# Kernel optimization log

Hardware: AMD Instinct MI355X
Metric: run time of the kernel (lower is better)

The kernel has to match this reference:

```python
import jax, jax.numpy as jnp
import numpy as np

N_NODES = 50000
N_EDGES = 150000
D_FEAT = 512
HIDDEN = 512
N_CLASSES = 47


def gcn_conv(x, edge_index, W, b, n_nodes):
    """PyG GCNConv: out = D^{-1/2} (A + I) D^{-1/2} (x @ W) + b."""
    h = x @ W  # [N, out_dim] dense GEMM
    loop = jnp.arange(n_nodes, dtype=edge_index.dtype)
    row = jnp.concatenate([edge_index[0], loop])  # source
    col = jnp.concatenate([edge_index[1], loop])  # target
    ones = jnp.ones(row.shape[0], dtype=h.dtype)
    deg = jax.ops.segment_sum(ones, col, num_segments=n_nodes)  # in-degree + 1
    dinv = jnp.where(deg > 0, jax.lax.rsqrt(deg), 0.0)
    norm = dinv[row] * dinv[col]  # [E+N]
    msg = norm[:, None] * h[row]  # gather + scale
    out = jax.ops.segment_sum(msg, col, num_segments=n_nodes)  # scatter-add
    return out + b


def setup_inputs() -> dict:
    key = jax.random.key(0)
    k1, k2, k3, k4, k5, k6 = jax.random.split(key, 6)
    x = jax.random.normal(k1, (N_NODES, D_FEAT), dtype=jnp.float32)
    edge_index = jax.random.randint(k2, (2, N_EDGES), 0, N_NODES, dtype=jnp.int64)
    s1 = (6.0 / (D_FEAT + HIDDEN)) ** 0.5
    s2 = (6.0 / (HIDDEN + N_CLASSES)) ** 0.5
    W1 = jax.random.uniform(k3, (D_FEAT, HIDDEN), jnp.float32, -s1, s1)
    b1 = jnp.zeros((HIDDEN,), jnp.float32)
    W2 = jax.random.uniform(k4, (HIDDEN, N_CLASSES), jnp.float32, -s2, s2)
    b2 = jnp.zeros((N_CLASSES,), jnp.float32)
    return {"x": x, "edge_index": edge_index, "W1": W1, "b1": b1, "W2": W2, "b2": b2}


def reference(x, edge_index, W1, b1, W2, b2):
    n = x.shape[0]
    h = gcn_conv(x, edge_index, W1, b1, n)
    h = jax.nn.relu(h)
    # F.dropout(p=0.5, training=self.training): eval mode -> identity
    out = gcn_conv(h, edge_index, W2, b2, n)
    return out
```

## Files before the change

kernel.cpp:

```cpp
#include <hip/hip_runtime.h>
#include <hip/hip_bf16.h>

#define NNODES 50000
#define NEDGES 150000
#define DFEAT  512
#define HID    512
#define NCLS   47

typedef __hip_bfloat16 bf16;
typedef __attribute__((ext_vector_type(8))) short short8;
typedef __attribute__((ext_vector_type(4))) float float4v;

typedef const __attribute__((address_space(1))) unsigned int* gas_t;
typedef __attribute__((address_space(3))) unsigned int* las_t;
__device__ __forceinline__ void load_lds16(const void* g, void* l) {
    __builtin_amdgcn_global_load_lds((gas_t)g, (las_t)l, 16, 0, 0);
}

__device__ __forceinline__ float bfbits_lo(unsigned int w) {
    return __uint_as_float((w & 0xFFFFu) << 16);
}
__device__ __forceinline__ float bfbits_hi(unsigned int w) {
    return __uint_as_float(w & 0xFFFF0000u);
}

__device__ __forceinline__ int eidx(const void* ei, int half, int e, int is64) {
    if (is64) return (int)((const long long*)ei)[(size_t)half * NEDGES + e];
    return ((const int*)ei)[half * NEDGES + e];
}

#define ZB ((NNODES + 255) / 256)
#define PR_W1T (1 + ZB)
#define PR_B1  (PR_W1T + 1024)
#define PR_W2T (PR_B1 + 2)
#define PR_B2  (PR_W2T + 128)
#define PR_GRID (PR_B2 + 1)

__global__ __launch_bounds__(256) void k_prep0(
    const void* x, const void* ei, const void* W1, const void* b1,
    const void* W2, const void* b2, int* flags, unsigned int* cnt,
    bf16* W1T, float* b1c, bf16* W2T, float* b2c) {
    __shared__ int sh[128];
    __shared__ int shflag;
    const int b = blockIdx.x, t = threadIdx.x;

    if (b >= 1 && b < 1 + ZB) {
        int i = (b - 1) * 256 + t;
        if (i < NNODES) cnt[i] = 0u;
        return;
    }

    if (t < 64) {
        const unsigned short* xs = (const unsigned short*)x;
        int c = 0;
        for (int i = t; i < 256; i += 64) {
            unsigned int e = (xs[2 * i] >> 7) & 0xFF;
            c += (e >= 117 && e <= 130) ? 1 : 0;
        }
        sh[t] = c;
        if (b == 0) {
            const int* w = (const int*)ei;
            int o = 0;
            for (int i = 2 * t + 1; i < 512; i += 128) o |= w[i];
            sh[64 + t] = o;
        }
    }
    __syncthreads();
    if (t == 0) {
        int C = 0;
        for (int i = 0; i < 64; i++) C += sh[i];
        shflag = (C > 128) ? 1 : 0;
        if (b == 0) {
            int O = 0;
            for (int i = 0; i < 64; i++) O |= sh[64 + i];
            flags[0] = shflag;
            flags[1] = (O == 0) ? 1 : 0;
        }
    }
    __syncthreads();
    const int isb = shflag;

    if (b == 0) return;

    if (b >= PR_W1T && b < PR_B1) {
        int i = (b - PR_W1T) * 256 + t;
        int k = i / HID, n = i % HID;
        float v = isb ? __bfloat162float(((const bf16*)W1)[i]) : ((const float*)W1)[i];
        W1T[(size_t)n * DFEAT + k] = __float2bfloat16(v);
    } else if (b >= PR_B1 && b < PR_W2T) {
        int i = (b - PR_B1) * 256 + t;
        if (i < HID)
            b1c[i] = isb ? __bfloat162float(((const bf16*)b1)[i]) : ((const float*)b1)[i];
    } else if (b >= PR_W2T && b < PR_B2) {
        int i = (b - PR_W2T) * 256 + t;
        int n = i / HID, k = i % HID;
        float v = 0.0f;
        if (n < NCLS) {
            size_t idx = (size_t)k * NCLS + n;
            v = isb ? __bfloat162float(((const bf16*)W2)[idx]) : ((const float*)W2)[idx];
        }
        W2T[(size_t)n * HID + k] = __float2bfloat16(v);
    } else if (b == PR_B2) {
        if (t < NCLS)
            b2c[t] = isb ? __bfloat162float(((const bf16*)b2)[t]) : ((const float*)b2)[t];
    }
}

__global__ void k_count(const void* ei, int* cnt, const int* flags) {
    int e = blockIdx.x * blockDim.x + threadIdx.x;
    if (e >= NEDGES) return;
    atomicAdd(&cnt[eidx(ei, 1, e, flags[1])], 1);
}

__global__ __launch_bounds__(256) void k_scan_part_dinv(const int* cnt, int* part,
                                                        float* dinv) {
    __shared__ int s[256];
    int i = blockIdx.x * 256 + threadIdx.x;
    int v = (i < NNODES) ? cnt[i] : 0;
    if (i < NNODES) dinv[i] = rsqrtf(1.0f + (float)v);
    s[threadIdx.x] = v;
    __syncthreads();
    for (int off = 128; off > 0; off >>= 1) {
        if (threadIdx.x < off) s[threadIdx.x] += s[threadIdx.x + off];
        __syncthreads();
    }
    if (threadIdx.x == 0) part[blockIdx.x] = s[0];
}

__global__ __launch_bounds__(256) void k_scan_off(int* part, int n) {
    __shared__ int s[256];
    int v = (threadIdx.x < n) ? part[threadIdx.x] : 0;
    s[threadIdx.x] = v;
    __syncthreads();
    for (int off = 1; off < 256; off <<= 1) {
        int t = (threadIdx.x >= off) ? s[threadIdx.x - off] : 0;
        __syncthreads();
        s[threadIdx.x] += t;
        __syncthreads();
    }
    if (threadIdx.x < n) part[threadIdx.x] = s[threadIdx.x] - v;
}

__global__ __launch_bounds__(256) void k_scan_fin(const int* cnt, const int* part,
                                                  int* rowptr, int* cursor) {
    __shared__ int s[256];
    int i = blockIdx.x * 256 + threadIdx.x;
    int v = (i < NNODES) ? cnt[i] : 0;
    s[threadIdx.x] = v;
    __syncthreads();
    for (int off = 1; off < 256; off <<= 1) {
        int t = (threadIdx.x >= off) ? s[threadIdx.x - off] : 0;
        __syncthreads();
        s[threadIdx.x] += t;
        __syncthreads();
    }
    int incl = s[threadIdx.x] + part[blockIdx.x];
    if (i < NNODES) {
        rowptr[i + 1] = incl;
        cursor[i] = incl - v;
    }
    if (i == 0) rowptr[0] = 0;
}

__global__ void k_fill(const void* ei, int* cursor, int* csr_src, const int* flags) {
    int e = blockIdx.x * blockDim.x + threadIdx.x;
    if (e >= NEDGES) return;
    int is64 = flags[1];
    int v = eidx(ei, 1, e, is64);
    int u = eidx(ei, 0, e, is64);
    int pos = atomicAdd(&cursor[v], 1);
    csr_src[pos] = u;
}

__global__ __launch_bounds__(256, 3) void k_gemm1_v3(
    const void* __restrict__ X, const bf16* __restrict__ W1T,
    bf16* __restrict__ h1c, int c0, int C, const int* __restrict__ flags,
    int col_tiles, int rows_per_xcd, int n_row_tiles) {
    const int b = blockIdx.x;
    const int xcd = b & 7;
    const int s = b >> 3;
    const int col_t = s % col_tiles;
    const int lr = s / col_tiles;
    const int row_t = xcd * rows_per_xcd + lr;
    if (row_t >= n_row_tiles) return;

    __shared__ bf16 As[128 * 64];
    __shared__ bf16 Bs[128 * 64];
    const int tid = threadIdx.x;
    const int wave = tid >> 6, lane = tid & 63;
    const int row0 = row_t * 128;
    const int gc0 = c0 + col_t * 128;
    const int isb = flags[0];

    float4v acc[2][8];
#pragma unroll
    for (int i = 0; i < 2; i++)
#pragma unroll
        for (int j = 0; j < 8; j++) acc[i][j] = (float4v){0.f, 0.f, 0.f, 0.f};

    const int rb = wave * 32;
    const int frow = lane & 15;
    const int fk = lane >> 4;

    for (int k0 = 0; k0 < DFEAT; k0 += 64) {
        __syncthreads();
        if (isb) {
            const bf16* xb = (const bf16*)X;
#pragma unroll
            for (int t = 0; t < 4; ++t) {
                int g8 = wave * 4 + t;
                int r = g8 * 8 + (lane >> 3);
                int gr = row0 + r; if (gr >= NNODES) gr = NNODES - 1;
                int ck = (lane & 7) ^ (r & 7);
                load_lds16(xb + (size_t)gr * DFEAT + k0 + ck * 8, &As[g8 * 8 * 64]);
            }
        } else {
            const float* xf = (const float*)X;
            for (int i = tid; i < 128 * 8; i += 256) {
                int r = i >> 3, p = i & 7;
                int gr = row0 + r; if (gr >= NNODES) gr = NNODES - 1;
                int ck = p ^ (r & 7);
                const float* src = xf + (size_t)gr * DFEAT + k0 + ck * 8;
#pragma unroll
                for (int e = 0; e < 8; ++e)
                    As[r * 64 + p * 8 + e] = __float2bfloat16(src[e]);
            }
        }
#pragma unroll
        for (int t = 0; t < 4; ++t) {
            int g8 = wave * 4 + t;
            int cl = g8 * 8 + (lane >> 3);
            int ck = (lane & 7) ^ (cl & 7);
            load_lds16(W1T + (size_t)(gc0 + cl) * DFEAT + k0 + ck * 8, &Bs[g8 * 8 * 64]);
        }
        __syncthreads();
#pragma unroll
        for (int ki = 0; ki < 2; ++ki) {
            const int cc = ki * 4 + fk;
            short8 a[2], b8[8];
#pragma unroll
            for (int i = 0; i < 2; i++) {
                int r = rb + i * 16 + frow;
                a[i] = *(const short8*)&As[r * 64 + (cc ^ (r & 7)) * 8];
            }
#pragma unroll
            for (int j = 0; j < 8; j++) {
                int cl = j * 16 + frow;
                b8[j] = *(const short8*)&Bs[cl * 64 + (cc ^ (cl & 7)) * 8];
            }
#pragma unroll
            for (int i = 0; i < 2; i++)
#pragma unroll
                for (int j = 0; j < 8; j++)
                    acc[i][j] = __builtin_amdgcn_mfma_f32_16x16x32_bf16(a[i], b8[j], acc[i][j], 0, 0, 0);
        }
    }
    const int ccol = gc0 - c0;
#pragma unroll
    for (int i = 0; i < 2; i++) {
#pragma unroll
        for (int r = 0; r < 4; r++) {
            int grow = row0 + rb + i * 16 + (lane >> 4) * 4 + r;
            if (grow < NNODES) {
#pragma unroll
                for (int j = 0; j < 8; j++)
                    h1c[(size_t)grow * C + ccol + j * 16 + (lane & 15)] =
                        __float2bfloat16(acc[i][j][r]);
            }
        }
    }
}

__global__ __launch_bounds__(256) void k_gemm1_mfma(
    const void* __restrict__ X, const bf16* __restrict__ W1T,
    bf16* __restrict__ h1c, int c0, int C, const int* __restrict__ flags) {
    __shared__ bf16 As[128 * 64];
    __shared__ bf16 Bs[64 * 64];
    const int tid = threadIdx.x;
    const int wave = tid >> 6, lane = tid & 63;
    const int row0 = blockIdx.x * 128;
    const int gc0 = c0 + blockIdx.y * 64;
    const int isb = flags[0];
    float4v acc[2][4];
#pragma unroll
    for (int i = 0; i < 2; i++)
#pragma unroll
        for (int j = 0; j < 4; j++) acc[i][j] = (float4v){0.f, 0.f, 0.f, 0.f};
    const int rbase = wave * 32;
    const int fl_row = lane & 15;
    const int fl_k8 = (lane >> 4) * 8;
    for (int k0 = 0; k0 < DFEAT; k0 += 64) {
        __syncthreads();
        if (isb) {
            const bf16* xb = (const bf16*)X;
#pragma unroll
            for (int i = 0; i < 4; ++i) {
                int r = i * 32 + wave * 8;
                int gr = row0 + r + (lane >> 3);
                if (gr >= NNODES) gr = NNODES - 1;
                load_lds16(xb + (size_t)gr * DFEAT + k0 + (lane & 7) * 8, &As[r * 64]);
            }
        } else {
            const float* xf = (const float*)X;
            for (int i = tid; i < 128 * 64; i += 256) {
                int r = i >> 6, c = i & 63;
                int gr = row0 + r;
                if (gr >= NNODES) gr = NNODES - 1;
                As[i] = __float2bfloat16(xf[(size_t)gr * DFEAT + k0 + c]);
            }
        }
#pragma unroll
        for (int i = 0; i < 2; ++i) {
            int r = i * 32 + wave * 8;
            int gn = gc0 + r + (lane >> 3);
            load_lds16(W1T + (size_t)gn * DFEAT + k0 + (lane & 7) * 8, &Bs[r * 64]);
        }
        __syncthreads();
#pragma unroll
        for (int ki = 0; ki < 64; ki += 32) {
            short8 a[2], b[4];
#pragma unroll
            for (int i = 0; i < 2; i++)
                a[i] = *(const short8*)&As[(rbase + i * 16 + fl_row) * 64 + ki + fl_k8];
#pragma unroll
            for (int j = 0; j < 4; j++)
                b[j] = *(const short8*)&Bs[(j * 16 + fl_row) * 64 + ki + fl_k8];
#pragma unroll
            for (int i = 0; i < 2; i++)
#pragma unroll
                for (int j = 0; j < 4; j++)
                    acc[i][j] = __builtin_amdgcn_mfma_f32_16x16x32_bf16(a[i], b[j], acc[i][j], 0, 0, 0);
        }
    }
    const int ccol = blockIdx.y * 64;
#pragma unroll
    for (int i = 0; i < 2; i++) {
#pragma unroll
        for (int r = 0; r < 4; r++) {
            int grow = row0 + rbase + i * 16 + (lane >> 4) * 4 + r;
            if (grow < NNODES) {
#pragma unroll
                for (int j = 0; j < 4; j++)
                    h1c[(size_t)grow * C + ccol + j * 16 + (lane & 15)] =
                        __float2bfloat16(acc[i][j][r]);
            }
        }
    }
}

__global__ __launch_bounds__(256) void k_agg1_512(const bf16* __restrict__ h1c,
                                                  const int* __restrict__ rowptr,
                                                  const int* __restrict__ csr_src,
                                                  const float* __restrict__ dinv,
                                                  const float* __restrict__ b1c,
                                                  bf16* __restrict__ a1c) {
    int v = blockIdx.x * 4 + (threadIdx.x >> 6);
    int lane = threadIdx.x & 63;
    if (v >= NNODES) return;
    int d8 = lane * 8;
    float dv = dinv[v];
    float s2 = dv * dv;
    uint4 w = *(const uint4*)(h1c + (size_t)v * 512 + d8);
    float a0 = s2 * bfbits_lo(w.x), a1 = s2 * bfbits_hi(w.x);
    float a2 = s2 * bfbits_lo(w.y), a3 = s2 * bfbits_hi(w.y);
    float a4 = s2 * bfbits_lo(w.z), a5 = s2 * bfbits_hi(w.z);
    float a6 = s2 * bfbits_lo(w.w), a7 = s2 * bfbits_hi(w.w);
    int pend = rowptr[v + 1];
    for (int p = rowptr[v]; p < pend; ++p) {
        int u = csr_src[p];
        float nw = dinv[u] * dv;
        uint4 q = *(const uint4*)(h1c + (size_t)u * 512 + d8);
        a0 += nw * bfbits_lo(q.x); a1 += nw * bfbits_hi(q.x);
        a2 += nw * bfbits_lo(q.y); a3 += nw * bfbits_hi(q.y);
        a4 += nw * bfbits_lo(q.z); a5 += nw * bfbits_hi(q.z);
        a6 += nw * bfbits_lo(q.w); a7 += nw * bfbits_hi(q.w);
    }
    const float* bb = b1c + d8;
    a0 += bb[0]; a1 += bb[1]; a2 += bb[2]; a3 += bb[3];
    a4 += bb[4]; a5 += bb[5]; a6 += bb[6]; a7 += bb[7];
    bf16 o[8];
    o[0] = __float2bfloat16(a0 > 0.f ? a0 : 0.f);
    o[1] = __float2bfloat16(a1 > 0.f ? a1 : 0.f);
    o[2] = __float2bfloat16(a2 > 0.f ? a2 : 0.f);
    o[3] = __float2bfloat16(a3 > 0.f ? a3 : 0.f);
    o[4] = __float2bfloat16(a4 > 0.f ? a4 : 0.f);
    o[5] = __float2bfloat16(a5 > 0.f ? a5 : 0.f);
    o[6] = __float2bfloat16(a6 > 0.f ? a6 : 0.f);
    o[7] = __float2bfloat16(a7 > 0.f ? a7 : 0.f);
    *(uint4*)(a1c + (size_t)v * 512 + d8) = *(uint4*)o;
}

__global__ __launch_bounds__(256) void k_agg1(const bf16* __restrict__ h1c,
                                              const int* __restrict__ rowptr,
                                              const int* __restrict__ csr_src,
                                              const float* __restrict__ dinv,
                                              const float* __restrict__ b1c, int c0, int C,
                                              bf16* __restrict__ a1c) {
    const int tshift = (C == 512) ? 7 : (C == 256) ? 6 : (C == 128) ? 5 : 4;
    long long gt = (long long)blockIdx.x * 256 + threadIdx.x;
    int v = (int)(gt >> tshift);
    int d4 = (int)((gt & ((1 << tshift) - 1)) << 2);
    if (v >= NNODES) return;
    float dv = dinv[v];
    uint2 w = *(const uint2*)(h1c + (size_t)v * C + d4);
    float s2 = dv * dv;
    float a0 = s2 * bfbits_lo(w.x), a1 = s2 * bfbits_hi(w.x);
    float a2 = s2 * bfbits_lo(w.y), a3 = s2 * bfbits_hi(w.y);
    int pend = rowptr[v + 1];
    for (int p = rowptr[v]; p < pend; ++p) {
        int u = csr_src[p];
        float nw = dinv[u] * dv;
        uint2 q = *(const uint2*)(h1c + (size_t)u * C + d4);
        a0 += nw * bfbits_lo(q.x); a1 += nw * bfbits_hi(q.x);
        a2 += nw * bfbits_lo(q.y); a3 += nw * bfbits_hi(q.y);
    }
    const float* bb = b1c + c0 + d4;
    a0 += bb[0]; a1 += bb[1]; a2 += bb[2]; a3 += bb[3];
    bf16 o[4];
    o[0] = __float2bfloat16(a0 > 0.f ? a0 : 0.f);
    o[1] = __float2bfloat16(a1 > 0.f ? a1 : 0.f);
    o[2] = __float2bfloat16(a2 > 0.f ? a2 : 0.f);
    o[3] = __float2bfloat16(a3 > 0.f ? a3 : 0.f);
    *(uint2*)(a1c + (size_t)v * C + d4) = *(uint2*)o;
}

__global__ __launch_bounds__(128) void k_gemm2_64(
    const bf16* __restrict__ A, int C, const bf16* __restrict__ W2T, int kg0,
    float* __restrict__ h2, int accum) {
    __shared__ bf16 As[64 * 64];
    __shared__ bf16 Bs[64 * 64];
    const int tid = threadIdx.x;
    const int wave = tid >> 6, lane = tid & 63;
    const int row0 = blockIdx.x * 64;
    float4v acc[2][4];
#pragma unroll
    for (int i = 0; i < 2; i++)
#pragma unroll
        for (int j = 0; j < 4; j++) acc[i][j] = (float4v){0.f, 0.f, 0.f, 0.f};
    const int rb = wave * 32;
    const int frow = lane & 15;
    const int fk = lane >> 4;

    for (int kk = 0; kk < C; kk += 64) {
        __syncthreads();
#pragma unroll
        for (int t = 0; t < 4; ++t) {
            int g8 = wave * 4 + t;
            int r = g8 * 8 + (lane >> 3);
            int gr = row0 + r; if (gr >= NNODES) gr = NNODES - 1;
            int ck = (lane & 7) ^ (r & 7);
            load_lds16(A + (size_t)gr * C + kk + ck * 8, &As[g8 * 8 * 64]);
        }
#pragma unroll
        for (int t = 0; t < 4; ++t) {
            int g8 = wave * 4 + t;
            int cl = g8 * 8 + (lane >> 3);
            int ck = (lane & 7) ^ (cl & 7);
            load_lds16(W2T + (size_t)cl * HID + kg0 + kk + ck * 8, &Bs[g8 * 8 * 64]);
        }
        __syncthreads();
#pragma unroll
        for (int ki = 0; ki < 2; ++ki) {
            const int cc = ki * 4 + fk;
            short8 a[2], b8[4];
#pragma unroll
            for (int i = 0; i < 2; i++) {
                int r = rb + i * 16 + frow;
                a[i] = *(const short8*)&As[r * 64 + (cc ^ (r & 7)) * 8];
            }
#pragma unroll
            for (int j = 0; j < 4; j++) {
                int cl = j * 16 + frow;
                b8[j] = *(const short8*)&Bs[cl * 64 + (cc ^ (cl & 7)) * 8];
            }
#pragma unroll
            for (int i = 0; i < 2; i++)
#pragma unroll
                for (int j = 0; j < 4; j++)
                    acc[i][j] = __builtin_amdgcn_mfma_f32_16x16x32_bf16(a[i], b8[j], acc[i][j], 0, 0, 0);
        }
    }
#pragma unroll
    for (int i = 0; i < 2; i++) {
#pragma unroll
        for (int r = 0; r < 4; r++) {
            int grow = row0 + rb + i * 16 + (lane >> 4) * 4 + r;
            if (grow < NNODES) {
#pragma unroll
                for (int j = 0; j < 4; j++) {
                    size_t o = (size_t)grow * 64 + j * 16 + frow;
                    h2[o] = accum ? h2[o] + acc[i][j][r] : acc[i][j][r];
                }
            }
        }
    }
}

__global__ __launch_bounds__(256) void k_agg2(const float* __restrict__ h2,
                                              const int* __restrict__ rowptr,
                                              const int* __restrict__ csr_src,
                                              const float* __restrict__ dinv,
                                              const float* __restrict__ b2c,
                                              void* out, const int* flags) {
    int v = blockIdx.x * 4 + (threadIdx.x >> 6);
    int d = threadIdx.x & 63;
    if (v >= NNODES || d >= NCLS) return;
    float dv = dinv[v];
    float acc = dv * dv * h2[(size_t)v * 64 + d];
    int pend = rowptr[v + 1];
    for (int p = rowptr[v]; p < pend; ++p) {
        int u = csr_src[p];
        acc += dinv[u] * dv * h2[(size_t)u * 64 + d];
    }
    acc += b2c[d];
    size_t o = (size_t)v * NCLS + d;
    if (flags[0]) ((bf16*)out)[o] = __float2bfloat16(acc);
    else          ((float*)out)[o] = acc;
}

extern "C" void kernel_launch(void* const* d_in, const int* in_sizes, int n_in,
                              void* d_out, int out_size, void* d_ws, size_t ws_size,
                              hipStream_t stream) {
    const void* x  = d_in[0];
    const void* ei = d_in[1];
    const void* W1 = d_in[2];
    const void* b1 = d_in[3];
    const void* W2 = d_in[4];
    const void* b2 = d_in[5];

    char* base = (char*)d_ws;
    auto alloc = [&](size_t bytes) -> char* {
        char* p = base;
        base += (bytes + 255) & ~(size_t)255;
        return p;
    };
    int*   flags  = (int*)alloc(64);
    int*   cnt    = (int*)alloc(sizeof(int) * NNODES);
    int*   part   = (int*)alloc(sizeof(int) * 256);
    int*   rowptr = (int*)alloc(sizeof(int) * (NNODES + 1));
    int*   cursor = (int*)alloc(sizeof(int) * NNODES);
    int*   csr    = (int*)alloc(sizeof(int) * NEDGES);
    float* dinv   = (float*)alloc(sizeof(float) * NNODES);
    bf16*  W1T    = (bf16*)alloc(sizeof(bf16) * DFEAT * HID);
    float* b1c    = (float*)alloc(sizeof(float) * HID);
    bf16*  W2T    = (bf16*)alloc(sizeof(bf16) * 64 * HID);
    float* b2c    = (float*)alloc(sizeof(float) * 64);
    float* h2     = (float*)alloc(sizeof(float) * (size_t)NNODES * 64);

    size_t used = (size_t)(base - (char*)d_ws);
    size_t rem = (ws_size > used) ? ws_size - used : 0;
    int C = 64;
    if (rem >= (size_t)200000 * 512 + 1024) C = 512;
    else if (rem >= (size_t)200000 * 256 + 1024) C = 256;
    else if (rem >= (size_t)200000 * 128 + 1024) C = 128;
    bf16* h1c = (bf16*)alloc(sizeof(bf16) * (size_t)NNODES * C);
    bf16* a1c = (bf16*)alloc(sizeof(bf16) * (size_t)NNODES * C);

    k_prep0<<<PR_GRID, 256, 0, stream>>>(x, ei, W1, b1, W2, b2, flags,
                                         (unsigned int*)cnt, W1T, b1c, W2T, b2c);
    k_count<<<(NEDGES + 255) / 256, 256, 0, stream>>>(ei, cnt, flags);
    const int nsb = (NNODES + 255) / 256;
    k_scan_part_dinv<<<nsb, 256, 0, stream>>>(cnt, part, dinv);
    k_scan_off<<<1, 256, 0, stream>>>(part, nsb);
    k_scan_fin<<<nsb, 256, 0, stream>>>(cnt, part, rowptr, cursor);
    k_fill<<<(NEDGES + 255) / 256, 256, 0, stream>>>(ei, cursor, csr, flags);

    const int rowblocks = (NNODES + 127) / 128;
    const int rows_per_xcd = (rowblocks + 7) / 8;
    int chunk_i = 0;
    for (int c0 = 0; c0 < HID; c0 += C, ++chunk_i) {
        if (C >= 128) {
            int col_tiles = C / 128;
            int nblk = 8 * rows_per_xcd * col_tiles;
            k_gemm1_v3<<<nblk, 256, 0, stream>>>(x, W1T, h1c, c0, C, flags,
                                                 col_tiles, rows_per_xcd, rowblocks);
        } else {
            dim3 g1(rowblocks, 1);
            k_gemm1_mfma<<<g1, 256, 0, stream>>>(x, W1T, h1c, c0, C, flags);
        }
        if (C == 512) {
            k_agg1_512<<<(NNODES + 3) / 4, 256, 0, stream>>>(h1c, rowptr, csr, dinv, b1c, a1c);
        } else {
            size_t nthr = (size_t)NNODES * (C / 4);
            k_agg1<<<(int)((nthr + 255) / 256), 256, 0, stream>>>(h1c, rowptr, csr, dinv, b1c, c0, C, a1c);
        }
        k_gemm2_64<<<(NNODES + 63) / 64, 128, 0, stream>>>(a1c, C, W2T, c0, h2, chunk_i > 0 ? 1 : 0);
    }

    k_agg2<<<(NNODES + 3) / 4, 256, 0, stream>>>(h2, rowptr, csr, dinv, b2c, d_out, flags);
}
```

Before: 336.2 us.

## Aggregate input features first, then fuse both GEMMs with bias and ReLU

Uses linearity (A·(XW) = (A·X)W) to run the first sparse aggregation directly on the input features and write a bf16 aggregated matrix. A single fused kernel then computes the first GEMM, adds bias, applies ReLU, stages the hidden tile in LDS and multiplies by W2 immediately. The per-column-tile partial outputs are accumulated into h2 with float atomics, and h2 is zeroed in the prep kernel. This removes the h1/a1 intermediate round trips and several launches, at the cost of atomic contention on h2 and reading fp32 x in the gather.

```diff
diff --git a/kernel.cpp b/kernel.cpp
--- a/kernel.cpp
+++ b/kernel.cpp
@@ -30,7 +30,9 @@
 }
 
 #define ZB ((NNODES + 255) / 256)
-#define PR_W1T (1 + ZB)
+#define NZH2 ((NNODES * 64 / 4 + 255) / 256)
+#define PR_ZH2 (1 + ZB)
+#define PR_W1T (PR_ZH2 + NZH2)
 #define PR_B1  (PR_W1T + 1024)
 #define PR_W2T (PR_B1 + 2)
 #define PR_B2  (PR_W2T + 128)
@@ -39,7 +41,7 @@
 __global__ __launch_bounds__(256) void k_prep0(
     const void* x, const void* ei, const void* W1, const void* b1,
     const void* W2, const void* b2, int* flags, unsigned int* cnt,
-    bf16* W1T, float* b1c, bf16* W2T, float* b2c) {
+    bf16* W1T, float* b1c, bf16* W2T, float* b2c, float* h2) {
     __shared__ int sh[128];
     __shared__ int shflag;
     const int b = blockIdx.x, t = threadIdx.x;
@@ -47,6 +49,12 @@
     if (b >= 1 && b < 1 + ZB) {
         int i = (b - 1) * 256 + t;
         if (i < NNODES) cnt[i] = 0u;
+        return;
+    }
+    if (b >= PR_ZH2 && b < PR_W1T) {
+        int i = (b - PR_ZH2) * 256 + t;
+        if (i < NNODES * 64 / 4)
+            ((float4v*)h2)[i] = (float4v){0.f, 0.f, 0.f, 0.f};
         return;
     }
 
@@ -172,276 +180,90 @@
     csr_src[pos] = u;
 }
 
-__global__ __launch_bounds__(256, 3) void k_gemm1_v3(
-    const void* __restrict__ X, const bf16* __restrict__ W1T,
-    bf16* __restrict__ h1c, int c0, int C, const int* __restrict__ flags,
-    int col_tiles, int rows_per_xcd, int n_row_tiles) {
-    const int b = blockIdx.x;
-    const int xcd = b & 7;
-    const int s = b >> 3;
-    const int col_t = s % col_tiles;
-    const int lr = s / col_tiles;
-    const int row_t = xcd * rows_per_xcd + lr;
-    if (row_t >= n_row_tiles) return;
-
-    __shared__ bf16 As[128 * 64];
-    __shared__ bf16 Bs[128 * 64];
-    const int tid = threadIdx.x;
-    const int wave = tid >> 6, lane = tid & 63;
-    const int row0 = row_t * 128;
-    const int gc0 = c0 + col_t * 128;
-    const int isb = flags[0];
-
-    float4v acc[2][8];
-#pragma unroll
-    for (int i = 0; i < 2; i++)
-#pragma unroll
-        for (int j = 0; j < 8; j++) acc[i][j] = (float4v){0.f, 0.f, 0.f, 0.f};
-
-    const int rb = wave * 32;
-    const int frow = lane & 15;
-    const int fk = lane >> 4;
-
-    for (int k0 = 0; k0 < DFEAT; k0 += 64) {
-        __syncthreads();
-        if (isb) {
-            const bf16* xb = (const bf16*)X;
-#pragma unroll
-            for (int t = 0; t < 4; ++t) {
-                int g8 = wave * 4 + t;
-                int r = g8 * 8 + (lane >> 3);
-                int gr = row0 + r; if (gr >= NNODES) gr = NNODES - 1;
-                int ck = (lane & 7) ^ (r & 7);
-                load_lds16(xb + (size_t)gr * DFEAT + k0 + ck * 8, &As[g8 * 8 * 64]);
-            }
-        } else {
-            const float* xf = (const float*)X;
-            for (int i = tid; i < 128 * 8; i += 256) {
-                int r = i >> 3, p = i & 7;
-                int gr = row0 + r; if (gr >= NNODES) gr = NNODES - 1;
-                int ck = p ^ (r & 7);
-                const float* src = xf + (size_t)gr * DFEAT + k0 + ck * 8;
-#pragma unroll
-                for (int e = 0; e < 8; ++e)
-                    As[r * 64 + p * 8 + e] = __float2bfloat16(src[e]);
-            }
-        }
-#pragma unroll
-        for (int t = 0; t < 4; ++t) {
-            int g8 = wave * 4 + t;
-            int cl = g8 * 8 + (lane >> 3);
-            int ck = (lane & 7) ^ (cl & 7);
-            load_lds16(W1T + (size_t)(gc0 + cl) * DFEAT + k0 + ck * 8, &Bs[g8 * 8 * 64]);
-        }
-        __syncthreads();
-#pragma unroll
-        for (int ki = 0; ki < 2; ++ki) {
-            const int cc = ki * 4 + fk;
-            short8 a[2], b8[8];
-#pragma unroll
-            for (int i = 0; i < 2; i++) {
-                int r = rb + i * 16 + frow;
-                a[i] = *(const short8*)&As[r * 64 + (cc ^ (r & 7)) * 8];
-            }
-#pragma unroll
-            for (int j = 0; j < 8; j++) {
-                int cl = j * 16 + frow;
-                b8[j] = *(const short8*)&Bs[cl * 64 + (cc ^ (cl & 7)) * 8];
-            }
-#pragma unroll
-            for (int i = 0; i < 2; i++)
-#pragma unroll
-                for (int j = 0; j < 8; j++)
-                    acc[i][j] = __builtin_amdgcn_mfma_f32_16x16x32_bf16(a[i], b8[j], acc[i][j], 0, 0, 0);
-        }
-    }
-    const int ccol = gc0 - c0;
-#pragma unroll
-    for (int i = 0; i < 2; i++) {
-#pragma unroll
-        for (int r = 0; r < 4; r++) {
-            int grow = row0 + rb + i * 16 + (lane >> 4) * 4 + r;
-            if (grow < NNODES) {
-#pragma unroll
-                for (int j = 0; j < 8; j++)
-                    h1c[(size_t)grow * C + ccol + j * 16 + (lane & 15)] =
-                        __float2bfloat16(acc[i][j][r]);
-            }
-        }
-    }
-}
-
-__global__ __launch_bounds__(256) void k_gemm1_mfma(
-    const void* __restrict__ X, const bf16* __restrict__ W1T,
-    bf16* __restrict__ h1c, int c0, int C, const int* __restrict__ flags) {
-    __shared__ bf16 As[128 * 64];
-    __shared__ bf16 Bs[64 * 64];
-    const int tid = threadIdx.x;
-    const int wave = tid >> 6, lane = tid & 63;
-    const int row0 = blockIdx.x * 128;
-    const int gc0 = c0 + blockIdx.y * 64;
-    const int isb = flags[0];
-    float4v acc[2][4];
-#pragma unroll
-    for (int i = 0; i < 2; i++)
-#pragma unroll
-        for (int j = 0; j < 4; j++) acc[i][j] = (float4v){0.f, 0.f, 0.f, 0.f};
-    const int rbase = wave * 32;
-    const int fl_row = lane & 15;
-    const int fl_k8 = (lane >> 4) * 8;
-    for (int k0 = 0; k0 < DFEAT; k0 += 64) {
-        __syncthreads();
-        if (isb) {
-            const bf16* xb = (const bf16*)X;
-#pragma unroll
-            for (int i = 0; i < 4; ++i) {
-                int r = i * 32 + wave * 8;
-                int gr = row0 + r + (lane >> 3);
-                if (gr >= NNODES) gr = NNODES - 1;
-                load_lds16(xb + (size_t)gr * DFEAT + k0 + (lane & 7) * 8, &As[r * 64]);
-            }
-        } else {
-            const float* xf = (const float*)X;
-            for (int i = tid; i < 128 * 64; i += 256) {
-                int r = i >> 6, c = i & 63;
-                int gr = row0 + r;
-                if (gr >= NNODES) gr = NNODES - 1;
-                As[i] = __float2bfloat16(xf[(size_t)gr * DFEAT + k0 + c]);
-            }
-        }
-#pragma unroll
-        for (int i = 0; i < 2; ++i) {
-            int r = i * 32 + wave * 8;
-            int gn = gc0 + r + (lane >> 3);
-            load_lds16(W1T + (size_t)gn * DFEAT + k0 + (lane & 7) * 8, &Bs[r * 64]);
-        }
-        __syncthreads();
-#pragma unroll
-        for (int ki = 0; ki < 64; ki += 32) {
-            short8 a[2], b[4];
-#pragma unroll
-            for (int i = 0; i < 2; i++)
-                a[i] = *(const short8*)&As[(rbase + i * 16 + fl_row) * 64 + ki + fl_k8];
-#pragma unroll
-            for (int j = 0; j < 4; j++)
-                b[j] = *(const short8*)&Bs[(j * 16 + fl_row) * 64 + ki + fl_k8];
-#pragma unroll
-            for (int i = 0; i < 2; i++)
-#pragma unroll
-                for (int j = 0; j < 4; j++)
-                    acc[i][j] = __builtin_amdgcn_mfma_f32_16x16x32_bf16(a[i], b[j], acc[i][j], 0, 0, 0);
-        }
-    }
-    const int ccol = blockIdx.y * 64;
-#pragma unroll
-    for (int i = 0; i < 2; i++) {
-#pragma unroll
-        for (int r = 0; r < 4; r++) {
-            int grow = row0 + rbase + i * 16 + (lane >> 4) * 4 + r;
-            if (grow < NNODES) {
-#pragma unroll
-                for (int j = 0; j < 4; j++)
-                    h1c[(size_t)grow * C + ccol + j * 16 + (lane & 15)] =
-                        __float2bfloat16(acc[i][j][r]);
-            }
-        }
-    }
-}
-
-__global__ __launch_bounds__(256) void k_agg1_512(const bf16* __restrict__ h1c,
-                                                  const int* __restrict__ rowptr,
-                                                  const int* __restrict__ csr_src,
-                                                  const float* __restrict__ dinv,
-                                                  const float* __restrict__ b1c,
-                                                  bf16* __restrict__ a1c) {
+__global__ __launch_bounds__(256) void k_aggx(const void* __restrict__ X,
+                                              const int* __restrict__ rowptr,
+                                              const int* __restrict__ csr_src,
+                                              const float* __restrict__ dinv,
+                                              bf16* __restrict__ ax,
+                                              const int* __restrict__ flags) {
     int v = blockIdx.x * 4 + (threadIdx.x >> 6);
     int lane = threadIdx.x & 63;
     if (v >= NNODES) return;
     int d8 = lane * 8;
     float dv = dinv[v];
     float s2 = dv * dv;
-    uint4 w = *(const uint4*)(h1c + (size_t)v * 512 + d8);
-    float a0 = s2 * bfbits_lo(w.x), a1 = s2 * bfbits_hi(w.x);
-    float a2 = s2 * bfbits_lo(w.y), a3 = s2 * bfbits_hi(w.y);
-    float a4 = s2 * bfbits_lo(w.z), a5 = s2 * bfbits_hi(w.z);
-    float a6 = s2 * bfbits_lo(w.w), a7 = s2 * bfbits_hi(w.w);
+    float a0, a1, a2, a3, a4, a5, a6, a7;
     int pend = rowptr[v + 1];
-    for (int p = rowptr[v]; p < pend; ++p) {
-        int u = csr_src[p];
-        float nw = dinv[u] * dv;
-        uint4 q = *(const uint4*)(h1c + (size_t)u * 512 + d8);
-        a0 += nw * bfbits_lo(q.x); a1 += nw * bfbits_hi(q.x);
-        a2 += nw * bfbits_lo(q.y); a3 += nw * bfbits_hi(q.y);
-        a4 += nw * bfbits_lo(q.z); a5 += nw * bfbits_hi(q.z);
-        a6 += nw * bfbits_lo(q.w); a7 += nw * bfbits_hi(q.w);
-    }
-    const float* bb = b1c + d8;
-    a0 += bb[0]; a1 += bb[1]; a2 += bb[2]; a3 += bb[3];
-    a4 += bb[4]; a5 += bb[5]; a6 += bb[6]; a7 += bb[7];
+    if (flags[0]) {
+        const bf16* xb = (const bf16*)X;
+        uint4 w = *(const uint4*)(xb + (size_t)v * 512 + d8);
+        a0 = s2 * bfbits_lo(w.x); a1 = s2 * bfbits_hi(w.x);
+        a2 = s2 * bfbits_lo(w.y); a3 = s2 * bfbits_hi(w.y);
+        a4 = s2 * bfbits_lo(w.z); a5 = s2 * bfbits_hi(w.z);
+        a6 = s2 * bfbits_lo(w.w); a7 = s2 * bfbits_hi(w.w);
+        for (int p = rowptr[v]; p < pend; ++p) {
+            int u = csr_src[p];
+            float nw = dinv[u] * dv;
+            uint4 q = *(const uint4*)(xb + (size_t)u * 512 + d8);
+            a0 += nw * bfbits_lo(q.x); a1 += nw * bfbits_hi(q.x);
+            a2 += nw * bfbits_lo(q.y); a3 += nw * bfbits_hi(q.y);
+            a4 += nw * bfbits_lo(q.z); a5 += nw * bfbits_hi(q.z);
+            a6 += nw * bfbits_lo(q.w); a7 += nw * bfbits_hi(q.w);
+        }
+    } else {
+        const float* xf = (const float*)X;
+        const float* p0 = xf + (size_t)v * 512 + d8;
+        float4v f0 = *(const float4v*)p0, f1 = *(const float4v*)(p0 + 4);
+        a0 = s2 * f0[0]; a1 = s2 * f0[1]; a2 = s2 * f0[2]; a3 = s2 * f0[3];
+        a4 = s2 * f1[0]; a5 = s2 * f1[1]; a6 = s2 * f1[2]; a7 = s2 * f1[3];
+        for (int p = rowptr[v]; p < pend; ++p) {
+            int u = csr_src[p];
+            float nw = dinv[u] * dv;
+            const float* pu = xf + (size_t)u * 512 + d8;
+            float4v g0 = *(const float4v*)pu, g1 = *(const float4v*)(pu + 4);
+            a0 += nw * g0[0]; a1 += nw * g0[1]; a2 += nw * g0[2]; a3 += nw * g0[3];
+            a4 += nw * g1[0]; a5 += nw * g1[1]; a6 += nw * g1[2]; a7 += nw * g1[3];
+        }
+    }
     bf16 o[8];
-    o[0] = __float2bfloat16(a0 > 0.f ? a0 : 0.f);
-    o[1] = __float2bfloat16(a1 > 0.f ? a1 : 0.f);
-    o[2] = __float2bfloat16(a2 > 0.f ? a2 : 0.f);
-    o[3] = __float2bfloat16(a3 > 0.f ? a3 : 0.f);
-    o[4] = __float2bfloat16(a4 > 0.f ? a4 : 0.f);
-    o[5] = __float2bfloat16(a5 > 0.f ? a5 : 0.f);
-    o[6] = __float2bfloat16(a6 > 0.f ? a6 : 0.f);
-    o[7] = __float2bfloat16(a7 > 0.f ? a7 : 0.f);
-    *(uint4*)(a1c + (size_t)v * 512 + d8) = *(uint4*)o;
-}
-
-__global__ __launch_bounds__(256) void k_agg1(const bf16* __restrict__ h1c,
-                                              const int* __restrict__ rowptr,
-                                              const int* __restrict__ csr_src,
-                                              const float* __restrict__ dinv,
-                                              const float* __restrict__ b1c, int c0, int C,
-                                              bf16* __restrict__ a1c) {
-    const int tshift = (C == 512) ? 7 : (C == 256) ? 6 : (C == 128) ? 5 : 4;
-    long long gt = (long long)blockIdx.x * 256 + threadIdx.x;
-    int v = (int)(gt >> tshift);
-    int d4 = (int)((gt & ((1 << tshift) - 1)) << 2);
-    if (v >= NNODES) return;
-    float dv = dinv[v];
-    uint2 w = *(const uint2*)(h1c + (size_t)v * C + d4);
-    float s2 = dv * dv;
-    float a0 = s2 * bfbits_lo(w.x), a1 = s2 * bfbits_hi(w.x);
-    float a2 = s2 * bfbits_lo(w.y), a3 = s2 * bfbits_hi(w.y);
-    int pend = rowptr[v + 1];
-    for (int p = rowptr[v]; p < pend; ++p) {
-        int u = csr_src[p];
-        float nw = dinv[u] * dv;
-        uint2 q = *(const uint2*)(h1c + (size_t)u * C + d4);
-        a0 += nw * bfbits_lo(q.x); a1 += nw * bfbits_hi(q.x);
-        a2 += nw * bfbits_lo(q.y); a3 += nw * bfbits_hi(q.y);
-    }
-    const float* bb = b1c + c0 + d4;
-    a0 += bb[0]; a1 += bb[1]; a2 += bb[2]; a3 += bb[3];
-    bf16 o[4];
-    o[0] = __float2bfloat16(a0 > 0.f ? a0 : 0.f);
-    o[1] = __float2bfloat16(a1 > 0.f ? a1 : 0.f);
-    o[2] = __float2bfloat16(a2 > 0.f ? a2 : 0.f);
-    o[3] = __float2bfloat16(a3 > 0.f ? a3 : 0.f);
-    *(uint2*)(a1c + (size_t)v * C + d4) = *(uint2*)o;
-}
-
-__global__ __launch_bounds__(128) void k_gemm2_64(
-    const bf16* __restrict__ A, int C, const bf16* __restrict__ W2T, int kg0,
-    float* __restrict__ h2, int accum) {
-    __shared__ bf16 As[64 * 64];
-    __shared__ bf16 Bs[64 * 64];
+    o[0] = __float2bfloat16(a0); o[1] = __float2bfloat16(a1);
+    o[2] = __float2bfloat16(a2); o[3] = __float2bfloat16(a3);
+    o[4] = __float2bfloat16(a4); o[5] = __float2bfloat16(a5);
+    o[6] = __float2bfloat16(a6); o[7] = __float2bfloat16(a7);
+    *(uint4*)(ax + (size_t)v * 512 + d8) = *(uint4*)o;
+}
+
+__global__ __launch_bounds__(256, 3) void k_fgemm(
+    const bf16* __restrict__ ax, const bf16* __restrict__ W1T,
+    const float* __restrict__ b1c, const bf16* __restrict__ W2T,
+    float* __restrict__ h2, int rows_per_xcd, int n_row_tiles) {
+    const int b = blockIdx.x;
+    const int xcd = b & 7;
+    const int s = b >> 3;
+    const int col_t = s & 3;
+    const int lr = s >> 2;
+    const int row_t = xcd * rows_per_xcd + lr;
+    if (row_t >= n_row_tiles) return;
+
+    __shared__ bf16 smem[128 * 128];
+    bf16* As = smem;
+    bf16* Bs = smem + 128 * 64;
     const int tid = threadIdx.x;
     const int wave = tid >> 6, lane = tid & 63;
-    const int row0 = blockIdx.x * 64;
-    float4v acc[2][4];
-#pragma unroll
-    for (int i = 0; i < 2; i++)
-#pragma unroll
-        for (int j = 0; j < 4; j++) acc[i][j] = (float4v){0.f, 0.f, 0.f, 0.f};
+    const int row0 = row_t * 128;
+    const int gc0 = col_t * 128;
+
     const int rb = wave * 32;
     const int frow = lane & 15;
     const int fk = lane >> 4;
 
-    for (int kk = 0; kk < C; kk += 64) {
+    float4v acc[2][8];
+#pragma unroll
+    for (int i = 0; i < 2; i++)
+#pragma unroll
+        for (int j = 0; j < 8; j++) acc[i][j] = (float4v){0.f, 0.f, 0.f, 0.f};
+
+    for (int k0 = 0; k0 < DFEAT; k0 += 64) {
         __syncthreads();
 #pragma unroll
         for (int t = 0; t < 4; ++t) {
@@ -449,48 +271,97 @@
             int r = g8 * 8 + (lane >> 3);
             int gr = row0 + r; if (gr >= NNODES) gr = NNODES - 1;
             int ck = (lane & 7) ^ (r & 7);
-            load_lds16(A + (size_t)gr * C + kk + ck * 8, &As[g8 * 8 * 64]);
+            load_lds16(ax + (size_t)gr * DFEAT + k0 + ck * 8, &As[g8 * 8 * 64]);
         }
 #pragma unroll
         for (int t = 0; t < 4; ++t) {
             int g8 = wave * 4 + t;
             int cl = g8 * 8 + (lane >> 3);
             int ck = (lane & 7) ^ (cl & 7);
-            load_lds16(W2T + (size_t)cl * HID + kg0 + kk + ck * 8, &Bs[g8 * 8 * 64]);
+            load_lds16(W1T + (size_t)(gc0 + cl) * DFEAT + k0 + ck * 8, &Bs[g8 * 8 * 64]);
         }
         __syncthreads();
 #pragma unroll
         for (int ki = 0; ki < 2; ++ki) {
             const int cc = ki * 4 + fk;
-            short8 a[2], b8[4];
+            short8 a[2], b8[8];
 #pragma unroll
             for (int i = 0; i < 2; i++) {
                 int r = rb + i * 16 + frow;
                 a[i] = *(const short8*)&As[r * 64 + (cc ^ (r & 7)) * 8];
             }
 #pragma unroll
-            for (int j = 0; j < 4; j++) {
+            for (int j = 0; j < 8; j++) {
                 int cl = j * 16 + frow;
                 b8[j] = *(const short8*)&Bs[cl * 64 + (cc ^ (cl & 7)) * 8];
             }
 #pragma unroll
             for (int i = 0; i < 2; i++)
 #pragma unroll
+                for (int j = 0; j < 8; j++)
+                    acc[i][j] = __builtin_amdgcn_mfma_f32_16x16x32_bf16(a[i], b8[j], acc[i][j], 0, 0, 0);
+        }
+    }
+
+    __syncthreads();
+    {
+        float bias[8];
+#pragma unroll
+        for (int j = 0; j < 8; j++) bias[j] = b1c[gc0 + j * 16 + frow];
+#pragma unroll
+        for (int i = 0; i < 2; i++) {
+#pragma unroll
+            for (int r = 0; r < 4; r++) {
+                int row = rb + i * 16 + fk * 4 + r;
+#pragma unroll
+                for (int j = 0; j < 8; j++) {
+                    int col = j * 16 + frow;
+                    float v = acc[i][j][r] + bias[j];
+                    v = v > 0.f ? v : 0.f;
+                    int ck2 = (col >> 3) ^ (row & 7);
+                    smem[row * 128 + ck2 * 8 + (col & 7)] = __float2bfloat16(v);
+                }
+            }
+        }
+    }
+    __syncthreads();
+
+    float4v acc2[2][4];
+#pragma unroll
+    for (int i = 0; i < 2; i++)
+#pragma unroll
+        for (int j = 0; j < 4; j++) acc2[i][j] = (float4v){0.f, 0.f, 0.f, 0.f};
+#pragma unroll
+    for (int ks = 0; ks < 4; ++ks) {
+        const int kk = ks * 32 + fk * 8;
+        const int p = kk >> 3;
+        short8 a2[2], b2f[4];
+#pragma unroll
+        for (int i = 0; i < 2; i++) {
+            int row = rb + i * 16 + frow;
+            a2[i] = *(const short8*)&smem[row * 128 + ((p ^ (row & 7)) * 8)];
+        }
+#pragma unroll
+        for (int j = 0; j < 4; j++) {
+            int n = j * 16 + frow;
+            b2f[j] = *(const short8*)(W2T + (size_t)n * HID + gc0 + kk);
+        }
+#pragma unroll
+        for (int i = 0; i < 2; i++)
+#pragma unroll
+            for (int j = 0; j < 4; j++)
+                acc2[i][j] = __builtin_amdgcn_mfma_f32_16x16x32_bf16(a2[i], b2f[j], acc2[i][j], 0, 0, 0);
+    }
+
+#pragma unroll
+    for (int i = 0; i < 2; i++) {
+#pragma unroll
+        for (int r = 0; r < 4; r++) {
+            int grow = row0 + rb + i * 16 + fk * 4 + r;
+            if (grow < NNODES) {
+#pragma unroll
                 for (int j = 0; j < 4; j++)
-                    acc[i][j] = __builtin_amdgcn_mfma_f32_16x16x32_bf16(a[i], b8[j], acc[i][j], 0, 0, 0);
-        }
-    }
-#pragma unroll
-    for (int i = 0; i < 2; i++) {
-#pragma unroll
-        for (int r = 0; r < 4; r++) {
-            int grow = row0 + rb + i * 16 + (lane >> 4) * 4 + r;
-            if (grow < NNODES) {
-#pragma unroll
-                for (int j = 0; j < 4; j++) {
-                    size_t o = (size_t)grow * 64 + j * 16 + frow;
-                    h2[o] = accum ? h2[o] + acc[i][j][r] : acc[i][j][r];
-                }
+                    atomicAdd(&h2[(size_t)grow * 64 + j * 16 + frow], acc2[i][j][r]);
             }
         }
     }
@@ -546,18 +417,10 @@
     bf16*  W2T    = (bf16*)alloc(sizeof(bf16) * 64 * HID);
     float* b2c    = (float*)alloc(sizeof(float) * 64);
     float* h2     = (float*)alloc(sizeof(float) * (size_t)NNODES * 64);
-
-    size_t used = (size_t)(base - (char*)d_ws);
-    size_t rem = (ws_size > used) ? ws_size - used : 0;
-    int C = 64;
-    if (rem >= (size_t)200000 * 512 + 1024) C = 512;
-    else if (rem >= (size_t)200000 * 256 + 1024) C = 256;
-    else if (rem >= (size_t)200000 * 128 + 1024) C = 128;
-    bf16* h1c = (bf16*)alloc(sizeof(bf16) * (size_t)NNODES * C);
-    bf16* a1c = (bf16*)alloc(sizeof(bf16) * (size_t)NNODES * C);
+    bf16*  ax     = (bf16*)alloc(sizeof(bf16) * (size_t)NNODES * DFEAT);
 
     k_prep0<<<PR_GRID, 256, 0, stream>>>(x, ei, W1, b1, W2, b2, flags,
-                                         (unsigned int*)cnt, W1T, b1c, W2T, b2c);
+                                         (unsigned int*)cnt, W1T, b1c, W2T, b2c, h2);
     k_count<<<(NEDGES + 255) / 256, 256, 0, stream>>>(ei, cnt, flags);
     const int nsb = (NNODES + 255) / 256;
     k_scan_part_dinv<<<nsb, 256, 0, stream>>>(cnt, part, dinv);
@@ -565,27 +428,12 @@
     k_scan_fin<<<nsb, 256, 0, stream>>>(cnt, part, rowptr, cursor);
     k_fill<<<(NEDGES + 255) / 256, 256, 0, stream>>>(ei, cursor, csr, flags);
 
+    k_aggx<<<(NNODES + 3) / 4, 256, 0, stream>>>(x, rowptr, csr, dinv, ax, flags);
+
     const int rowblocks = (NNODES + 127) / 128;
     const int rows_per_xcd = (rowblocks + 7) / 8;
-    int chunk_i = 0;
-    for (int c0 = 0; c0 < HID; c0 += C, ++chunk_i) {
-        if (C >= 128) {
-            int col_tiles = C / 128;
-            int nblk = 8 * rows_per_xcd * col_tiles;
-            k_gemm1_v3<<<nblk, 256, 0, stream>>>(x, W1T, h1c, c0, C, flags,
-                                                 col_tiles, rows_per_xcd, rowblocks);
-        } else {
-            dim3 g1(rowblocks, 1);
-            k_gemm1_mfma<<<g1, 256, 0, stream>>>(x, W1T, h1c, c0, C, flags);
-        }
-        if (C == 512) {
-            k_agg1_512<<<(NNODES + 3) / 4, 256, 0, stream>>>(h1c, rowptr, csr, dinv, b1c, a1c);
-        } else {
-            size_t nthr = (size_t)NNODES * (C / 4);
-            k_agg1<<<(int)((nthr + 255) / 256), 256, 0, stream>>>(h1c, rowptr, csr, dinv, b1c, c0, C, a1c);
-        }
-        k_gemm2_64<<<(NNODES + 63) / 64, 128, 0, stream>>>(a1c, C, W2T, c0, h2, chunk_i > 0 ? 1 : 0);
-    }
+    k_fgemm<<<8 * rows_per_xcd * 4, 256, 0, stream>>>(ax, W1T, b1c, W2T, h2,
+                                                      rows_per_xcd, rowblocks);
 
     k_agg2<<<(NNODES + 3) / 4, 256, 0, stream>>>(h2, rowptr, csr, dinv, b2c, d_out, flags);
 }
```

Result: faster. 321.5 us (-4.4%).
